# Optimization experiments

Measured on AMD Instinct MI355X. Metric: run time of the kernel, lower is better.

Reference implementation:

```python
import jax, jax.numpy as jnp
import numpy as np

NEG_SLOPE = 0.1

def mlp(x, w1, b1, w2, b2):
    # MLP(sizes): Linear -> LeakyReLU(0.1) -> Linear
    return jax.nn.leaky_relu(x @ w1 + b1, NEG_SLOPE) @ w2 + b2

def _seg_mean(vals, idx, n):
    s = jax.ops.segment_sum(vals, idx, num_segments=n)
    cnt = jax.ops.segment_sum(jnp.ones((vals.shape[0],), vals.dtype), idx, num_segments=n)
    return s / jnp.maximum(cnt, 1.0)[:, None]

def setup_inputs() -> dict:
    key = jax.random.key(0)
    ks = iter(jax.random.split(key, 40))
    N, F, H, E = 100000, 64, 128, 800000
    Ha = H // 2  # hidden_dim/2 = 64
    def lin(k, i, o):
        k1, k2 = jax.random.split(k)
        return (jax.random.normal(k1, (i, o), jnp.float32) * (1.0 / np.sqrt(i)),
                jax.random.normal(k2, (o,), jnp.float32) * 0.01)
    inp = {}
    inp['feat'] = jax.random.normal(next(ks), (N, F), jnp.float32)
    inp['pi_feat'] = jax.random.normal(next(ks), (N, 4), jnp.float32)
    inp['level'] = jax.random.uniform(next(ks), (N, 1), jnp.float32)
    inp['bit_position'] = jax.random.uniform(next(ks), (E, 1), jnp.float32)
    inp['is_po'] = jax.random.randint(next(ks), (N,), 0, 2, jnp.int32)
    inp['is_module'] = jax.random.randint(next(ks), (N,), 0, 2, jnp.int32)
    inp['src_m'] = jax.random.randint(next(ks), (E,), 0, N, jnp.int32)
    inp['dst_m'] = jax.random.randint(next(ks), (E,), 0, N, jnp.int32)
    inp['src_g'] = jax.random.randint(next(ks), (E,), 0, N, jnp.int32)
    inp['dst_g'] = jax.random.randint(next(ks), (E,), 0, N, jnp.int32)
    # mlp_pi: 4 -> H/2 -> H
    inp['pi_w1'], inp['pi_b1'] = lin(next(ks), 4, Ha)
    inp['pi_w2'], inp['pi_b2'] = lin(next(ks), Ha, H)
    # mlp_neigh_module: H + F + 1 -> H/2 -> H
    inp['nm_w1'], inp['nm_b1'] = lin(next(ks), H + F + 1, Ha)
    inp['nm_w2'], inp['nm_b2'] = lin(next(ks), Ha, H)
    # mlp_neigh_gate: H + F -> H/2 -> H
    inp['ng_w1'], inp['ng_b1'] = lin(next(ks), H + F, Ha)
    inp['ng_w2'], inp['ng_b2'] = lin(next(ks), Ha, H)
    # mlp_global: 1 -> H/2 -> H
    inp['g_w1'], inp['g_b1'] = lin(next(ks), 1, Ha)
    inp['g_w2'], inp['g_b2'] = lin(next(ks), Ha, H)
    # mlp_out: 2H -> H -> 1
    inp['o_w1'], inp['o_b1'] = lin(next(ks), 2 * H, H)
    inp['o_w2'], inp['o_b2'] = lin(next(ks), H, 1)
    return inp

def reference(feat, pi_feat, level, bit_position,
              pi_w1, pi_b1, pi_w2, pi_b2,
              nm_w1, nm_b1, nm_w2, nm_b2,
              ng_w1, ng_b1, ng_w2, ng_b2,
              g_w1, g_b1, g_w2, g_b2,
              o_w1, o_b1, o_w2, o_b2,
              is_po, is_module, src_m, dst_m, src_g, dst_g):
    N = feat.shape[0]
    # PI init embedding (mlp_pi)
    h0 = mlp(pi_feat, pi_w1, pi_b1, pi_w2, pi_b2)            # [N, H]
    # module-edge message passing: m = src h, pos = bit_position; mean reduce
    m = h0[src_m]                                            # [E, H] irregular gather
    neigh_m = _seg_mean(m, dst_m, N)                         # [N, H]
    pos_m = _seg_mean(bit_position, dst_m, N)                # [N, 1]
    # nodes_func_module, agg_choice==0: cat(neigh, pos, feat) -> mlp_neigh_module
    h_m = mlp(jnp.concatenate([neigh_m, pos_m, feat], axis=1), nm_w1, nm_b1, nm_w2, nm_b2)
    # gate-edge message passing
    neigh_g = _seg_mean(h0[src_g], dst_g, N)                 # [N, H]
    h_g = mlp(jnp.concatenate([neigh_g, feat], axis=1), ng_w1, ng_b1, ng_w2, ng_b2)
    # ReLU on non-PO nodes only
    keep = (is_po != 1)[:, None]
    h_m = jnp.where(keep, jax.nn.relu(h_m), h_m)
    h_g = jnp.where(keep, jax.nn.relu(h_g), h_g)
    # per-node-type update (hetero apply_nodes)
    h = jnp.where((is_module == 1)[:, None], h_m, h_g)       # [N, H]
    # global branch + readout
    hg = mlp(level, g_w1, g_b1, g_w2, g_b2)                  # [N, H]
    out = mlp(jnp.concatenate([h, hg], axis=1), o_w1, o_b1, o_w2, o_b2)  # [N, 1]
    return out
```

## Files before the change

kernel.cpp:

```cpp
#include <hip/hip_runtime.h>

typedef __bf16 bf16x8 __attribute__((ext_vector_type(8)));
typedef float f32x4 __attribute__((ext_vector_type(4)));
typedef unsigned short u16;
typedef unsigned int u32;
typedef unsigned long long u64;

__device__ __forceinline__ u16 f2b(float f) {
  return __builtin_bit_cast(u16, (__bf16)f);
}
__device__ __forceinline__ float b2f_lo(u32 pk) {
  return __builtin_bit_cast(float, pk << 16);
}
__device__ __forceinline__ float b2f_hi(u32 pk) {
  return __builtin_bit_cast(float, pk & 0xffff0000u);
}
__device__ __forceinline__ float leaky(float x) { return x > 0.f ? x : 0.1f * x; }
__device__ __forceinline__ f32x4 mfma16(bf16x8 a, bf16x8 b, f32x4 c) {
  return __builtin_amdgcn_mfma_f32_16x16x32_bf16(a, b, c, 0, 0, 0);
}

#define P64 72
#define P128 136
#define CAP 16
#define RSTRIDE 48
#define RSTRIDE8 24

__global__ __launch_bounds__(256) void k_prep(
    const float* nm_w1, const float* ng_w1, const float* nm_w2, const float* ng_w2,
    const float* o_w1, const float* o_b1, const float* g_w2, const float* g_b2,
    const float* pi_w2, const float* pi_b2, const int* is_module,
    u16* wt_yc, float* bias_y, u16* wt_f1m, u16* wt_f1g, float* w_pos,
    u16* wt2m, u16* wt2g, u16* wt_oh, u16* gt, float* bp, u32* mbits, int N) {
  int i = blockIdx.x * 256 + threadIdx.x;
  if (i < 9216) {
    int ty = i / 4608, rem = i % 4608, n = rem / P64, k = rem % P64;
    float v = 0.f;
    if (k < 64) {
      const float* w1 = ty ? ng_w1 : nm_w1;
      for (int t = 0; t < 128; t++) v += pi_w2[k * 128 + t] * w1[t * 64 + n];
    }
    wt_yc[i] = f2b(v);
    return;
  }
  i -= 9216;
  if (i < 128) {
    int ty = i >> 6, n = i & 63;
    const float* w1 = ty ? ng_w1 : nm_w1;
    float v = 0.f;
    for (int t = 0; t < 128; t++) v += pi_b2[t] * w1[t * 64 + n];
    bias_y[i] = v;
    return;
  }
  i -= 128;
  if (i < 4608) {
    int n = i / P64, k = i % P64;
    wt_f1m[i] = f2b(k < 64 ? nm_w1[(129 + k) * 64 + n] : 0.f);
    return;
  }
  i -= 4608;
  if (i < 4608) {
    int n = i / P64, k = i % P64;
    wt_f1g[i] = f2b(k < 64 ? ng_w1[(128 + k) * 64 + n] : 0.f);
    return;
  }
  i -= 4608;
  if (i < 64) { w_pos[i] = nm_w1[128 * 64 + i]; return; }
  i -= 64;
  if (i < 9216) {
    int n = i / P64, k = i % P64;
    wt2m[i] = f2b(k < 64 ? nm_w2[k * 128 + n] : 0.f);
    return;
  }
  i -= 9216;
  if (i < 9216) {
    int n = i / P64, k = i % P64;
    wt2g[i] = f2b(k < 64 ? ng_w2[k * 128 + n] : 0.f);
    return;
  }
  i -= 9216;
  if (i < 17408) {
    int n = i / P128, k = i % P128;
    wt_oh[i] = f2b(k < 128 ? o_w1[k * 128 + n] : 0.f);
    return;
  }
  i -= 17408;
  if (i < 9216) {
    int n = i / P64, k = i % P64;
    float v = 0.f;
    if (k < 64)
      for (int t = 0; t < 128; t++) v += g_w2[k * 128 + t] * o_w1[(128 + t) * 128 + n];
    gt[i] = f2b(v);
    return;
  }
  i -= 9216;
  if (i < 128) {
    float s = o_b1[i];
    for (int t = 0; t < 128; t++) s += g_b2[t] * o_w1[(128 + t) * 128 + i];
    bp[i] = s;
    return;
  }
  i -= 128;
  {
    int n = i;
    int lane = threadIdx.x & 63;
    bool v = (n < N) && (is_module[n] == 1);
    u64 b = __ballot(v);
    if (lane == 0 && n < N) mbits[n >> 5] = (u32)b;
    if (lane == 32 && n < N) mbits[n >> 5] = (u32)(b >> 32);
  }
}

__global__ void k_scatter(const int* src_m, const int* dst_m, const int* src_g,
                          const int* dst_g, const u32* mbits, const float* bitpos,
                          int* rec, u64* spill, int* spillcnt, int E) {
  int e = blockIdx.x * 256 + threadIdx.x;
  u64* rec8 = (u64*)rec;
  if (e < E) {
    int d = dst_m[e];
    if ((mbits[d >> 5] >> (d & 31)) & 1) {
      int c = atomicAdd(&rec[d * RSTRIDE], 1);
      int s = src_m[e];
      float bpv = bitpos[e];
      if (c < CAP) {
        rec8[(size_t)d * RSTRIDE8 + 1 + c] =
            ((u64)(u32)s << 32) | (u64)__builtin_bit_cast(u32, bpv);
      } else {
        int p = atomicAdd(spillcnt, 1);
        spill[p] = ((u64)(u32)d << 32) | (u32)s;
        atomicAdd((float*)&rec[d * RSTRIDE + 1], bpv);
      }
    }
  } else if (e < 2 * E) {
    int d = dst_g[e - E];
    if (!((mbits[d >> 5] >> (d & 31)) & 1)) {
      int c = atomicAdd(&rec[d * RSTRIDE], 1);
      int s = src_g[e - E];
      if (c < CAP) {
        rec8[(size_t)d * RSTRIDE8 + 1 + c] = ((u64)(u32)s << 32);
      } else {
        int p = atomicAdd(spillcnt, 1);
        spill[p] = ((u64)(u32)d << 32) | (u32)s;
      }
    }
  }
}

__global__ __launch_bounds__(512) void k_pre(const float* pf, const float* feat,
                                             const float* pi_w1, const float* pi_b1,
                                             const u16* wt_yc_g, const float* bias_y,
                                             const u16* wt_f1m_g, const u16* wt_f1g_g,
                                             const float* nm_b1, const float* ng_b1,
                                             const u32* mbits,
                                             u16* y0, u16* f1, int N) {
  __shared__ __align__(16) u16 wyc[2][64 * P64];
  __shared__ __align__(16) u16 wf[2][64 * P64];
  __shared__ __align__(16) u16 tbuf[8][16 * P64];
  for (int i = threadIdx.x; i < 2304; i += 512) {
    ((u32*)wyc[0])[i] = ((const u32*)wt_yc_g)[i];
    ((u32*)wyc[1])[i] = ((const u32*)wt_yc_g)[2304 + i];
    ((u32*)wf[0])[i] = ((const u32*)wt_f1m_g)[i];
    ((u32*)wf[1])[i] = ((const u32*)wt_f1g_g)[i];
  }

  int lane = threadIdx.x & 63, wv = threadIdx.x >> 6;
  int lid = lane & 15, q = lane >> 4;

  bf16x8 w1f[4];
#pragma unroll
  for (int nt = 0; nt < 4; nt++) {
    bf16x8 f;
#pragma unroll
    for (int j = 0; j < 8; j++) {
      int k = q * 8 + j;
      f[j] = (__bf16)((k < 4) ? pi_w1[k * 64 + nt * 16 + lid] : 0.f);
    }
    w1f[nt] = f;
  }
  __syncthreads();

  int nbat = (N + 15) >> 4;
  for (int b0 = blockIdx.x * 8; b0 < nbat; b0 += gridDim.x * 8) {
    int b = b0 + wv;
    int batch = b < nbat ? b : nbat - 1;
    int id = batch * 16 + lid;
    if (id >= N) id = N - 1;

    bf16x8 a;
#pragma unroll
    for (int j = 0; j < 8; j++)
      a[j] = (__bf16)((q == 0 && j < 4) ? pf[(size_t)id * 4 + j] : 0.f);
    f32x4 z1[4];
#pragma unroll
    for (int nt = 0; nt < 4; nt++) {
      f32x4 c = {0.f, 0.f, 0.f, 0.f};
      z1[nt] = mfma16(a, w1f[nt], c);
    }
    __syncthreads();
#pragma unroll
    for (int nt = 0; nt < 4; nt++) {
      float bb = pi_b1[nt * 16 + lid];
#pragma unroll
      for (int r = 0; r < 4; r++)
        tbuf[wv][(q * 4 + r) * P64 + nt * 16 + lid] = f2b(leaky(z1[nt][r] + bb));
    }
    __syncthreads();
    bf16x8 a20 = *(const bf16x8*)&tbuf[wv][lid * P64 + q * 8];
    bf16x8 a21 = *(const bf16x8*)&tbuf[wv][lid * P64 + 32 + q * 8];

    int idr_[4];
#pragma unroll
    for (int r = 0; r < 4; r++) {
      int ii = batch * 16 + q * 4 + r;
      idr_[r] = ii < N ? ii : N - 1;
    }

#pragma unroll
    for (int ty = 0; ty < 2; ty++) {
#pragma unroll
      for (int nt = 0; nt < 4; nt++) {
        f32x4 c = {0.f, 0.f, 0.f, 0.f};
        c = mfma16(a20, *(const bf16x8*)&wyc[ty][(nt * 16 + lid) * P64 + q * 8], c);
        c = mfma16(a21, *(const bf16x8*)&wyc[ty][(nt * 16 + lid) * P64 + 32 + q * 8], c);
        float by = bias_y[ty * 64 + nt * 16 + lid];
#pragma unroll
        for (int r = 0; r < 4; r++)
          y0[(size_t)idr_[r] * 128 + ty * 64 + nt * 16 + lid] = f2b(c[r] + by);
      }
    }

    bf16x8 af[2];
#pragma unroll
    for (int kt = 0; kt < 2; kt++) {
      const float4* p = (const float4*)(feat + (size_t)id * 64 + kt * 32 + q * 8);
      float4 xa = p[0], xb = p[1];
      bf16x8 f;
      f[0] = (__bf16)xa.x; f[1] = (__bf16)xa.y; f[2] = (__bf16)xa.z; f[3] = (__bf16)xa.w;
      f[4] = (__bf16)xb.x; f[5] = (__bf16)xb.y; f[6] = (__bf16)xb.z; f[7] = (__bf16)xb.w;
      af[kt] = f;
    }
#pragma unroll
    for (int nt = 0; nt < 4; nt++) {
      f32x4 cm = {0.f, 0.f, 0.f, 0.f}, cg = {0.f, 0.f, 0.f, 0.f};
#pragma unroll
      for (int kt = 0; kt < 2; kt++) {
        cm = mfma16(af[kt], *(const bf16x8*)&wf[0][(nt * 16 + lid) * P64 + kt * 32 + q * 8], cm);
        cg = mfma16(af[kt], *(const bf16x8*)&wf[1][(nt * 16 + lid) * P64 + kt * 32 + q * 8], cg);
      }
      float bm = nm_b1[nt * 16 + lid], bg = ng_b1[nt * 16 + lid];
#pragma unroll
      for (int r = 0; r < 4; r++) {
        int idr = idr_[r];
        bool mod = (mbits[idr >> 5] >> (idr & 31)) & 1;
        f1[(size_t)idr * 64 + nt * 16 + lid] = f2b(mod ? cm[r] + bm : cg[r] + bg);
      }
    }
  }
}

__global__ __launch_bounds__(256) void k_gather(const u16* y0, const int* rec,
                                                const u64* spill, const int* spillcnt,
                                                const u32* mbits, const u16* f1,
                                                const float* w_pos, u16* z1a, int N) {
  int n = (blockIdx.x * 256 + threadIdx.x) >> 6;
  int lane = threadIdx.x & 63;
  if (n >= N) return;
  bool mod = (mbits[n >> 5] >> (n & 31)) & 1;
  int sub = lane >> 5, l32 = lane & 31;
  int rv = (lane < 34) ? rec[(size_t)n * RSTRIDE + lane] : 0;
  int cnt = __shfl(rv, 0);
  float pspill = __builtin_bit_cast(float, __shfl(rv, 1));
  int inl = cnt < CAP ? cnt : CAP;
  float myb = 0.f;
  if (mod && lane >= 2 && lane < 34 && !(lane & 1) && ((lane - 2) >> 1) < inl)
    myb = __builtin_bit_cast(float, rv);
  const u32* yrow = (const u32*)y0;
  int halfo = mod ? 0 : 32;
  float a0 = 0.f, a1 = 0.f;
  for (int j = 0; j < inl; j += 2) {
    int e2 = j + sub;
    if (e2 < inl) {
      int s = __shfl(rv, 3 + 2 * e2);
      u32 pk = yrow[(size_t)s * 64 + halfo + l32];
      a0 += b2f_lo(pk);
      a1 += b2f_hi(pk);
    }
  }
  if (cnt > CAP) {
    int sc = *spillcnt;
    for (int base = 0; base < sc; base += 64) {
      int i = base + lane;
      u64 ent = (i < sc) ? spill[i] : 0xffffffffffffffffull;
      bool m = ((int)(ent >> 32) == n);
      u64 bal = __ballot(m);
      int slo = (int)(ent & 0xffffffffu);
      while (bal) {
        int l = __ffsll((long long)bal) - 1;
        bal &= bal - 1;
        int s = __shfl(slo, l);
        if (sub == 0) {
          u32 pk = yrow[(size_t)s * 64 + halfo + l32];
          a0 += b2f_lo(pk);
          a1 += b2f_hi(pk);
        }
      }
    }
  }
  a0 += __shfl_xor(a0, 32);
  a1 += __shfl_xor(a1, 32);
#pragma unroll
  for (int off = 1; off < 64; off <<= 1) myb += __shfl_xor(myb, off);
  float psum = pspill + myb;
  float inv = 1.f / (float)(cnt > 1 ? cnt : 1);
  if (sub == 0) {
    u32 fp = ((const u32*)f1)[(size_t)n * 32 + l32];
    float z0 = a0 * inv + b2f_lo(fp);
    float z1v = a1 * inv + b2f_hi(fp);
    if (mod) {
      float pm = psum * inv;
      float2 wp = ((const float2*)w_pos)[l32];
      z0 += pm * wp.x;
      z1v += pm * wp.y;
    }
    ((u32*)z1a)[(size_t)n * 32 + l32] = (u32)f2b(leaky(z0)) | ((u32)f2b(leaky(z1v)) << 16);
  }
}

__global__ __launch_bounds__(512) void k_tail(const u16* z1a, const u16* wt2m_g,
                                              const u16* wt2g_g, const float* nm_b2,
                                              const float* ng_b2, const u32* mbits,
                                              const int* is_po, const float* level,
                                              const float* g_w1, const float* g_b1,
                                              const u16* wt_oh_g, const u16* gt_g,
                                              const float* bp_g, const float* o_w2,
                                              const float* o_b2, float* out, int N) {
  __shared__ __align__(16) u16 w2[2][128 * P64];
  __shared__ __align__(16) u16 wt_oh[128 * P128];
  __shared__ __align__(16) u16 gt[128 * P64];
  __shared__ __align__(16) u16 tbuf[8][16 * P128];
  for (int i = threadIdx.x; i < 128 * P64 / 2; i += 512) {
    ((u32*)w2[0])[i] = ((const u32*)wt2m_g)[i];
    ((u32*)w2[1])[i] = ((const u32*)wt2g_g)[i];
    ((u32*)gt)[i] = ((const u32*)gt_g)[i];
  }
  for (int i = threadIdx.x; i < 128 * P128 / 2; i += 512)
    ((u32*)wt_oh)[i] = ((const u32*)wt_oh_g)[i];

  int lane = threadIdx.x & 63, wv = threadIdx.x >> 6;
  int lid = lane & 15, q = lane >> 4;
  int nbat = (N + 15) >> 4;

  float gw[2][8], gb[2][8];
#pragma unroll
  for (int kt = 0; kt < 2; kt++)
#pragma unroll
    for (int j = 0; j < 8; j++) {
      int k = kt * 32 + q * 8 + j;
      gw[kt][j] = g_w1[k];
      gb[kt][j] = g_b1[k];
    }
  float w2o[8], bpv[8];
#pragma unroll
  for (int nt = 0; nt < 8; nt++) {
    w2o[nt] = o_w2[nt * 16 + lid];
    bpv[nt] = bp_g[nt * 16 + lid];
  }
  float b2m[8], b2g[8];
#pragma unroll
  for (int nt = 0; nt < 8; nt++) {
    b2m[nt] = nm_b2[nt * 16 + lid];
    b2g[nt] = ng_b2[nt * 16 + lid];
  }
  float ob2 = o_b2[0];
  __syncthreads();

  for (int b0 = blockIdx.x * 8; b0 < nbat; b0 += gridDim.x * 8) {
    int b = b0 + wv;
    int batch = b < nbat ? b : nbat - 1;
    int id = batch * 16 + lid;
    if (id >= N) id = N - 1;

    bf16x8 a0 = *(const bf16x8*)(z1a + (size_t)id * 64 + q * 8);
    bf16x8 a1 = *(const bf16x8*)(z1a + (size_t)id * 64 + 32 + q * 8);
    bool mod_[4], kp_[4];
#pragma unroll
    for (int r = 0; r < 4; r++) {
      int ii = batch * 16 + q * 4 + r;
      if (ii >= N) ii = N - 1;
      mod_[r] = (mbits[ii >> 5] >> (ii & 31)) & 1;
      kp_[r] = (is_po[ii] != 1);
    }
    __syncthreads();
#pragma unroll
    for (int nt = 0; nt < 8; nt++) {
      f32x4 cm = {0.f, 0.f, 0.f, 0.f}, cg = {0.f, 0.f, 0.f, 0.f};
      cm = mfma16(a0, *(const bf16x8*)&w2[0][(nt * 16 + lid) * P64 + q * 8], cm);
      cm = mfma16(a1, *(const bf16x8*)&w2[0][(nt * 16 + lid) * P64 + 32 + q * 8], cm);
      cg = mfma16(a0, *(const bf16x8*)&w2[1][(nt * 16 + lid) * P64 + q * 8], cg);
      cg = mfma16(a1, *(const bf16x8*)&w2[1][(nt * 16 + lid) * P64 + 32 + q * 8], cg);
#pragma unroll
      for (int r = 0; r < 4; r++) {
        float v = mod_[r] ? cm[r] + b2m[nt] : cg[r] + b2g[nt];
        if (kp_[r]) v = fmaxf(v, 0.f);
        tbuf[wv][(q * 4 + r) * P128 + nt * 16 + lid] = f2b(v);
      }
    }
    __syncthreads();

    bf16x8 ah[4];
#pragma unroll
    for (int kt = 0; kt < 4; kt++)
      ah[kt] = *(const bf16x8*)&tbuf[wv][lid * P128 + kt * 32 + q * 8];
    float lv = level[id];
    bf16x8 ag[2];
#pragma unroll
    for (int kt = 0; kt < 2; kt++)
#pragma unroll
      for (int j = 0; j < 8; j++)
        ag[kt][j] = (__bf16)leaky(lv * gw[kt][j] + gb[kt][j]);

    f32x4 accv[8];
#pragma unroll
    for (int nt = 0; nt < 8; nt++) {
      f32x4 c = {0.f, 0.f, 0.f, 0.f};
#pragma unroll
      for (int kt = 0; kt < 4; kt++)
        c = mfma16(ah[kt], *(const bf16x8*)&wt_oh[(nt * 16 + lid) * P128 + kt * 32 + q * 8], c);
#pragma unroll
      for (int kt = 0; kt < 2; kt++)
        c = mfma16(ag[kt], *(const bf16x8*)&gt[(nt * 16 + lid) * P64 + kt * 32 + q * 8], c);
      accv[nt] = c;
    }
    float p[4];
#pragma unroll
    for (int r = 0; r < 4; r++) {
      float s = 0.f;
#pragma unroll
      for (int nt = 0; nt < 8; nt++) s += leaky(accv[nt][r] + bpv[nt]) * w2o[nt];
      p[r] = s;
    }
#pragma unroll
    for (int r = 0; r < 4; r++)
#pragma unroll
      for (int off = 1; off < 16; off <<= 1) p[r] += __shfl_xor(p[r], off, 16);
    if (lid == 0) {
#pragma unroll
      for (int r = 0; r < 4; r++) {
        int idr = batch * 16 + q * 4 + r;
        if (idr >= N) idr = N - 1;
        out[idr] = p[r] + ob2;
      }
    }
  }
}

extern "C" void kernel_launch(void* const* d_in, const int* in_sizes, int n_in,
                              void* d_out, int out_size, void* d_ws, size_t ws_size,
                              hipStream_t stream) {
  const float* feat = (const float*)d_in[0];
  const float* pi_feat = (const float*)d_in[1];
  const float* level = (const float*)d_in[2];
  const float* bitpos = (const float*)d_in[3];
  const int* is_po = (const int*)d_in[4];
  const int* is_module = (const int*)d_in[5];
  const int* src_m = (const int*)d_in[6];
  const int* dst_m = (const int*)d_in[7];
  const int* src_g = (const int*)d_in[8];
  const int* dst_g = (const int*)d_in[9];
  const float* pi_w1 = (const float*)d_in[10];
  const float* pi_b1 = (const float*)d_in[11];
  const float* pi_w2 = (const float*)d_in[12];
  const float* pi_b2 = (const float*)d_in[13];
  const float* nm_w1 = (const float*)d_in[14];
  const float* nm_b1 = (const float*)d_in[15];
  const float* nm_w2 = (const float*)d_in[16];
  const float* nm_b2 = (const float*)d_in[17];
  const float* ng_w1 = (const float*)d_in[18];
  const float* ng_b1 = (const float*)d_in[19];
  const float* ng_w2 = (const float*)d_in[20];
  const float* ng_b2 = (const float*)d_in[21];
  const float* g_w1 = (const float*)d_in[22];
  const float* g_b1 = (const float*)d_in[23];
  const float* g_w2 = (const float*)d_in[24];
  const float* g_b2 = (const float*)d_in[25];
  const float* o_w1 = (const float*)d_in[26];
  const float* o_b1 = (const float*)d_in[27];
  const float* o_w2 = (const float*)d_in[28];
  const float* o_b2 = (const float*)d_in[29];

  int N = in_sizes[0] / 64;
  int E = in_sizes[3];

  char* ws = (char*)d_ws;
  size_t off = 0;
  auto alloc = [&](size_t bytes) {
    char* p = ws + off;
    off += (bytes + 255) & ~(size_t)255;
    return p;
  };
  int* rec = (int*)alloc(((size_t)N * RSTRIDE + 64) * 4);
  int* spillcnt = (int*)alloc(16);
  size_t zero_bytes = off;
  u64* spill = (u64*)alloc((size_t)2 * E * 8);
  u32* mbits = (u32*)alloc((size_t)((N + 31) / 32) * 4);
  u16* y0 = (u16*)alloc((size_t)N * 128 * 2);
  u16* f1 = (u16*)alloc((size_t)N * 64 * 2);
  u16* z1a = (u16*)alloc((size_t)N * 64 * 2);
  u16* wt_yc = (u16*)alloc(9216 * 2);
  float* bias_y = (float*)alloc(128 * 4);
  u16* wt_f1m = (u16*)alloc(4608 * 2);
  u16* wt_f1g = (u16*)alloc(4608 * 2);
  float* w_pos = (float*)alloc(64 * 4);
  u16* wt2m = (u16*)alloc(9216 * 2);
  u16* wt2g = (u16*)alloc(9216 * 2);
  u16* wt_oh = (u16*)alloc(17408 * 2);
  u16* gt = (u16*)alloc(9216 * 2);
  float* bp = (float*)alloc(128 * 4);

  hipMemsetAsync(rec, 0, zero_bytes, stream);

  int prep_items = 63808 + ((N + 63) & ~63);
  k_prep<<<(prep_items + 255) / 256, 256, 0, stream>>>(
      nm_w1, ng_w1, nm_w2, ng_w2, o_w1, o_b1, g_w2, g_b2, pi_w2, pi_b2, is_module,
      wt_yc, bias_y, wt_f1m, wt_f1g, w_pos, wt2m, wt2g, wt_oh, gt, bp, mbits, N);

  k_scatter<<<(2 * E + 255) / 256, 256, 0, stream>>>(src_m, dst_m, src_g, dst_g,
                                                     mbits, bitpos, rec, spill,
                                                     spillcnt, E);

  k_pre<<<512, 512, 0, stream>>>(
      pi_feat, feat, pi_w1, pi_b1, wt_yc, bias_y, wt_f1m, wt_f1g,
      nm_b1, ng_b1, mbits, y0, f1, N);

  k_gather<<<(N * 64 + 255) / 256, 256, 0, stream>>>(
      y0, rec, spill, spillcnt, mbits, f1, w_pos, z1a, N);

  k_tail<<<256, 512, 0, stream>>>(z1a, wt2m, wt2g, nm_b2, ng_b2, mbits, is_po,
                                  level, g_w1, g_b1, wt_oh, gt, bp, o_w2, o_b2,
                                  (float*)d_out, N);
}
```

Before: 277.3 us.

## Fuse edge scatter and node pre-MLP into one kernel with block specialization

Merges the edge-scatter kernel and the per-node pre-processing kernel into a single launch. The first 384 blocks grid-stride over all edges doing the atomic bucketing, and the remaining 128 blocks run the pre-MLP over node batches. The two independent stages can then overlap on the device and one launch boundary disappears. In exchange, the pre-MLP gets far fewer blocks, and scatter blocks carry the large shared-memory footprint of the pre-MLP, which may limit occupancy for the atomic-heavy scatter.

Result: no change. 280.6 us (+1.2%).

```diff
diff --git a/kernel.cpp b/kernel.cpp
--- a/kernel.cpp
+++ b/kernel.cpp
@@ -25,6 +25,7 @@
 #define CAP 16
 #define RSTRIDE 48
 #define RSTRIDE8 24
+#define SCB 384
 
 __global__ __launch_bounds__(256) void k_prep(
     const float* nm_w1, const float* ng_w1, const float* nm_w2, const float* ng_w2,
@@ -111,51 +112,55 @@
   }
 }
 
-__global__ void k_scatter(const int* src_m, const int* dst_m, const int* src_g,
-                          const int* dst_g, const u32* mbits, const float* bitpos,
-                          int* rec, u64* spill, int* spillcnt, int E) {
-  int e = blockIdx.x * 256 + threadIdx.x;
-  u64* rec8 = (u64*)rec;
-  if (e < E) {
-    int d = dst_m[e];
-    if ((mbits[d >> 5] >> (d & 31)) & 1) {
-      int c = atomicAdd(&rec[d * RSTRIDE], 1);
-      int s = src_m[e];
-      float bpv = bitpos[e];
-      if (c < CAP) {
-        rec8[(size_t)d * RSTRIDE8 + 1 + c] =
-            ((u64)(u32)s << 32) | (u64)__builtin_bit_cast(u32, bpv);
-      } else {
-        int p = atomicAdd(spillcnt, 1);
-        spill[p] = ((u64)(u32)d << 32) | (u32)s;
-        atomicAdd((float*)&rec[d * RSTRIDE + 1], bpv);
-      }
-    }
-  } else if (e < 2 * E) {
-    int d = dst_g[e - E];
-    if (!((mbits[d >> 5] >> (d & 31)) & 1)) {
-      int c = atomicAdd(&rec[d * RSTRIDE], 1);
-      int s = src_g[e - E];
-      if (c < CAP) {
-        rec8[(size_t)d * RSTRIDE8 + 1 + c] = ((u64)(u32)s << 32);
-      } else {
-        int p = atomicAdd(spillcnt, 1);
-        spill[p] = ((u64)(u32)d << 32) | (u32)s;
-      }
-    }
-  }
-}
-
-__global__ __launch_bounds__(512) void k_pre(const float* pf, const float* feat,
-                                             const float* pi_w1, const float* pi_b1,
-                                             const u16* wt_yc_g, const float* bias_y,
-                                             const u16* wt_f1m_g, const u16* wt_f1g_g,
-                                             const float* nm_b1, const float* ng_b1,
-                                             const u32* mbits,
-                                             u16* y0, u16* f1, int N) {
+__global__ __launch_bounds__(512) void k_scpre(
+    const int* src_m, const int* dst_m, const int* src_g, const int* dst_g,
+    const float* bitpos, int* rec, u64* spill, int* spillcnt, int E,
+    const float* pf, const float* feat, const float* pi_w1, const float* pi_b1,
+    const u16* wt_yc_g, const float* bias_y, const u16* wt_f1m_g,
+    const u16* wt_f1g_g, const float* nm_b1, const float* ng_b1,
+    const u32* mbits, u16* y0, u16* f1, int N) {
   __shared__ __align__(16) u16 wyc[2][64 * P64];
   __shared__ __align__(16) u16 wf[2][64 * P64];
   __shared__ __align__(16) u16 tbuf[8][16 * P64];
+
+  if (blockIdx.x < SCB) {
+    u64* rec8 = (u64*)rec;
+    int stride = SCB * 512;
+    for (int e = blockIdx.x * 512 + threadIdx.x; e < 2 * E; e += stride) {
+      if (e < E) {
+        int d = dst_m[e];
+        if ((mbits[d >> 5] >> (d & 31)) & 1) {
+          int c = atomicAdd(&rec[d * RSTRIDE], 1);
+          int s = src_m[e];
+          float bpv = bitpos[e];
+          if (c < CAP) {
+            rec8[(size_t)d * RSTRIDE8 + 1 + c] =
+                ((u64)(u32)s << 32) | (u64)__builtin_bit_cast(u32, bpv);
+          } else {
+            int p = atomicAdd(spillcnt, 1);
+            spill[p] = ((u64)(u32)d << 32) | (u32)s;
+            atomicAdd((float*)&rec[d * RSTRIDE + 1], bpv);
+          }
+        }
+      } else {
+        int d = dst_g[e - E];
+        if (!((mbits[d >> 5] >> (d & 31)) & 1)) {
+          int c = atomicAdd(&rec[d * RSTRIDE], 1);
+          int s = src_g[e - E];
+          if (c < CAP) {
+            rec8[(size_t)d * RSTRIDE8 + 1 + c] = ((u64)(u32)s << 32);
+          } else {
+            int p = atomicAdd(spillcnt, 1);
+            spill[p] = ((u64)(u32)d << 32) | (u32)s;
+          }
+        }
+      }
+    }
+    return;
+  }
+
+  int pb = blockIdx.x - SCB;
+  int PB = gridDim.x - SCB;
   for (int i = threadIdx.x; i < 2304; i += 512) {
     ((u32*)wyc[0])[i] = ((const u32*)wt_yc_g)[i];
     ((u32*)wyc[1])[i] = ((const u32*)wt_yc_g)[2304 + i];
@@ -180,7 +185,7 @@
   __syncthreads();
 
   int nbat = (N + 15) >> 4;
-  for (int b0 = blockIdx.x * 8; b0 < nbat; b0 += gridDim.x * 8) {
+  for (int b0 = pb * 8; b0 < nbat; b0 += PB * 8) {
     int b = b0 + wv;
     int batch = b < nbat ? b : nbat - 1;
     int id = batch * 16 + lid;
@@ -524,11 +529,8 @@
       nm_w1, ng_w1, nm_w2, ng_w2, o_w1, o_b1, g_w2, g_b2, pi_w2, pi_b2, is_module,
       wt_yc, bias_y, wt_f1m, wt_f1g, w_pos, wt2m, wt2g, wt_oh, gt, bp, mbits, N);
 
-  k_scatter<<<(2 * E + 255) / 256, 256, 0, stream>>>(src_m, dst_m, src_g, dst_g,
-                                                     mbits, bitpos, rec, spill,
-                                                     spillcnt, E);
-
-  k_pre<<<512, 512, 0, stream>>>(
+  k_scpre<<<512, 512, 0, stream>>>(
+      src_m, dst_m, src_g, dst_g, bitpos, rec, spill, spillcnt, E,
       pi_feat, feat, pi_w1, pi_b1, wt_yc, bias_y, wt_f1m, wt_f1g,
       nm_b1, ng_b1, mbits, y0, f1, N);
 
```
